# Optimization experiments

Hardware: AMD Instinct MI355X
Metric: run time of the kernel (lower is better)

## Reference

```python
import jax, jax.numpy as jnp
import numpy as np

B, JX, JM, D, H = 8, 2048, 2048, 512, 512
NEG_INF = -1e30


def setup_inputs() -> dict:
    key = jax.random.key(0)
    ks = jax.random.split(key, 6)
    inputs = jax.random.normal(ks[0], (B, JX, D), dtype=jnp.float32)
    memory = jax.random.normal(ks[1], (B, JM, D), dtype=jnp.float32)
    mask = jax.random.randint(ks[2], (B, JM), 0, 2, dtype=jnp.int32)
    # guarantee at least one valid memory slot per row
    mask = mask.at[:, 0].set(1)
    Wq = jax.random.normal(ks[3], (D, H), dtype=jnp.float32) * 0.05
    Wk = jax.random.normal(ks[4], (D, H), dtype=jnp.float32) * 0.05
    Wg = jax.random.normal(ks[5], (2 * D, 2 * D), dtype=jnp.float32) * 0.05
    return {"inputs": inputs, "memory": memory, "mask": mask,
            "Wq": Wq, "Wk": Wk, "Wg": Wg}


def reference(inputs, memory, mask, Wq, Wk, Wg):
    hidden = Wq.shape[-1]
    # two ReLU projections (no bias)
    q = jax.nn.relu(jnp.einsum('bxd,dh->bxh', inputs, Wq))   # [B,JX,H]
    k = jax.nn.relu(jnp.einsum('bmd,dh->bmh', memory, Wk))   # [B,JM,H]
    # scaled dot-product scores
    scores = jnp.einsum('bxh,bmh->bxm', q, k) / (hidden ** 0.5)  # [B,JX,JM]
    # softmax_mask: -inf where mask == 0 (broadcast over JX instead of tile)
    m = mask[:, None, :].astype(scores.dtype)                 # [B,1,JM]
    scores = scores * m + (1.0 - m) * NEG_INF
    logits = jax.nn.softmax(scores, axis=-1)                  # [B,JX,JM]
    # attend over RAW memory (not projected)
    att = jnp.einsum('bxm,bmd->bxd', logits, memory)          # [B,JX,D]
    # gate combiner: concat -> dense(sigmoid, no bias) -> multiply
    res = jnp.concatenate([inputs, att], axis=-1)             # [B,JX,2D]
    g = jax.nn.sigmoid(jnp.einsum('bxe,ef->bxf', res, Wg))
    return res * g
```

## Files before the change

kernel.cpp:

```cpp
#include <hip/hip_runtime.h>

typedef unsigned short u16;
typedef unsigned int   u32;

typedef short s16x8 __attribute__((ext_vector_type(8)));
typedef float f32x4 __attribute__((ext_vector_type(4)));

static __device__ __forceinline__ u16 f2bf(float f) {
  u32 u = __float_as_uint(f);
  u = (u + 0x7fffu + ((u >> 16) & 1u)) >> 16;
  return (u16)u;
}
static __device__ __forceinline__ float bf2f(u16 h) {
  return __uint_as_float(((u32)h) << 16);
}
static __device__ __forceinline__ f32x4 mfma16(s16x8 a, s16x8 b, f32x4 c) {
  return __builtin_amdgcn_mfma_f32_16x16x32_bf16(a, b, c, 0, 0, 0);
}
static __device__ __forceinline__ void gload16(const u16* g, u16* l) {
  __builtin_amdgcn_global_load_lds(
      (const __attribute__((address_space(1))) void*)g,
      (__attribute__((address_space(3))) void*)l, 16, 0, 0);
}

__global__ __launch_bounds__(256) void cvt_k(const float* __restrict__ in,
                                             u16* __restrict__ out, int n8) {
  int i = blockIdx.x * 256 + threadIdx.x;
  if (i >= n8) return;
  const float4* p = reinterpret_cast<const float4*>(in);
  float4 a = p[2 * i], b = p[2 * i + 1];
  union { u16 u[8]; uint4 v; } r;
  r.u[0] = f2bf(a.x); r.u[1] = f2bf(a.y); r.u[2] = f2bf(a.z); r.u[3] = f2bf(a.w);
  r.u[4] = f2bf(b.x); r.u[5] = f2bf(b.y); r.u[6] = f2bf(b.z); r.u[7] = f2bf(b.w);
  reinterpret_cast<uint4*>(out)[i] = r.v;
}

__global__ void tcvt_k(const float* __restrict__ in, u16* __restrict__ out,
                       int R, int C, long long ibs, long long obs) {
  __shared__ float t[32][33];
  const float* ip = in + (size_t)blockIdx.z * ibs;
  u16* op = out + (size_t)blockIdx.z * obs;
  int r0 = blockIdx.y * 32, c0 = blockIdx.x * 32;
  int x = threadIdx.x, y = threadIdx.y;
  for (int i = y; i < 32; i += 8) t[i][x] = ip[(size_t)(r0 + i) * C + c0 + x];
  __syncthreads();
  for (int i = y; i < 32; i += 8) op[(size_t)(c0 + i) * R + r0 + x] = f2bf(t[x][i]);
}

__global__ __launch_bounds__(256) void softmax_k(u16* __restrict__ P,
                                                 const int* __restrict__ mask,
                                                 float scale) {
  __shared__ float redm[4], reds[4];
  const int row = blockIdx.x;
  const int bb = row >> 11;
  const int tid = threadIdx.x;
  u16* p = P + (size_t)row * 2048;
  const int* mk = mask + (size_t)bb * 2048;
  uint4 raw = reinterpret_cast<const uint4*>(p)[tid];
  int4 ma = reinterpret_cast<const int4*>(mk)[2 * tid];
  int4 mc = reinterpret_cast<const int4*>(mk)[2 * tid + 1];
  float v[8];
  v[0] = ma.x ? bf2f((u16)(raw.x & 0xffff)) * scale : -1e30f;
  v[1] = ma.y ? bf2f((u16)(raw.x >> 16))    * scale : -1e30f;
  v[2] = ma.z ? bf2f((u16)(raw.y & 0xffff)) * scale : -1e30f;
  v[3] = ma.w ? bf2f((u16)(raw.y >> 16))    * scale : -1e30f;
  v[4] = mc.x ? bf2f((u16)(raw.z & 0xffff)) * scale : -1e30f;
  v[5] = mc.y ? bf2f((u16)(raw.z >> 16))    * scale : -1e30f;
  v[6] = mc.z ? bf2f((u16)(raw.w & 0xffff)) * scale : -1e30f;
  v[7] = mc.w ? bf2f((u16)(raw.w >> 16))    * scale : -1e30f;
  float mx = v[0];
  #pragma unroll
  for (int i = 1; i < 8; ++i) mx = fmaxf(mx, v[i]);
  for (int off = 32; off; off >>= 1) mx = fmaxf(mx, __shfl_xor(mx, off));
  if ((tid & 63) == 0) redm[tid >> 6] = mx;
  __syncthreads();
  mx = fmaxf(fmaxf(redm[0], redm[1]), fmaxf(redm[2], redm[3]));
  float sum = 0.f;
  #pragma unroll
  for (int i = 0; i < 8; ++i) { v[i] = __expf(v[i] - mx); sum += v[i]; }
  for (int off = 32; off; off >>= 1) sum += __shfl_xor(sum, off);
  if ((tid & 63) == 0) reds[tid >> 6] = sum;
  __syncthreads();
  sum = reds[0] + reds[1] + reds[2] + reds[3];
  float inv = 1.0f / sum;
  union { u16 u[8]; uint4 q; } r;
  #pragma unroll
  for (int i = 0; i < 8; ++i) r.u[i] = f2bf(v[i] * inv);
  reinterpret_cast<uint4*>(p)[tid] = r.q;
}

template <int EPI, int NT, int NX, int NY,
          int LDA, int LDB, int LDC, int KSPLIT, int MSPLIT,
          long long ABS, long long BBS, long long CBS, int NWG>
__global__ __launch_bounds__(256) void g128(
    const u16* __restrict__ A, const u16* __restrict__ A2,
    const u16* __restrict__ Bt, const u16* __restrict__ Bt2,
    float* __restrict__ Cf, u16* __restrict__ Cb,
    const float* __restrict__ R0, const u16* __restrict__ R1) {
  __shared__ u16 As[128 * 64];
  __shared__ u16 Bs[128 * 64];
  const int bid = blockIdx.x;
  const int wgid = (bid & 7) * (NWG / 8) + (bid >> 3);
  const int bx = wgid % NX;
  const int by = (wgid / NX) % NY;
  const int bz = wgid / (NX * NY);
  const int tid = threadIdx.x;
  const int wave = tid >> 6, lane = tid & 63;
  const int m0 = by * 128, n0 = bx * 128;
  const int wr = wave >> 1, wc = wave & 1;
  const int l15 = lane & 15, l4 = lane >> 4;
  const int srow = lane >> 3;
  const int scolsw = (((lane & 7) ^ (lane >> 3)) << 3);
  const int rsw = (l15 & 7) << 3;
  const u16* Bbase = ((m0 < MSPLIT) ? Bt : Bt2) + (size_t)bz * BBS;

  f32x4 acc[4][4];
  #pragma unroll
  for (int i = 0; i < 4; ++i)
    #pragma unroll
    for (int j = 0; j < 4; ++j) acc[i][j] = (f32x4){0.f, 0.f, 0.f, 0.f};

  for (int t = 0; t < NT; ++t) {
    const int k0 = t * 64;
    const u16* Ab;
    int kl;
    if (k0 < KSPLIT) { Ab = A + (size_t)bz * ABS;  kl = k0; }
    else             { Ab = A2 + (size_t)bz * ABS; kl = k0 - KSPLIT; }
    __syncthreads();
    #pragma unroll
    for (int c = 0; c < 4; ++c) {
      int chunk = wave * 4 + c;
      int row = chunk * 8 + srow;
      gload16(Ab + (size_t)(m0 + row) * LDA + kl + scolsw, &As[chunk * 512]);
      gload16(Bbase + (size_t)(n0 + row) * LDB + k0 + scolsw, &Bs[chunk * 512]);
    }
    __syncthreads();
    #pragma unroll
    for (int kk = 0; kk < 64; kk += 32) {
      s16x8 af[4], bfr[4];
      #pragma unroll
      for (int mi = 0; mi < 4; ++mi)
        af[mi] = *reinterpret_cast<const s16x8*>(
            &As[(wr * 64 + mi * 16 + l15) * 64 + ((kk + l4 * 8) ^ rsw)]);
      #pragma unroll
      for (int ni = 0; ni < 4; ++ni)
        bfr[ni] = *reinterpret_cast<const s16x8*>(
            &Bs[(wc * 64 + ni * 16 + l15) * 64 + ((kk + l4 * 8) ^ rsw)]);
      #pragma unroll
      for (int mi = 0; mi < 4; ++mi)
        #pragma unroll
        for (int ni = 0; ni < 4; ++ni)
          acc[mi][ni] = mfma16(af[mi], bfr[ni], acc[mi][ni]);
    }
  }

  #pragma unroll
  for (int mi = 0; mi < 4; ++mi) {
    #pragma unroll
    for (int ni = 0; ni < 4; ++ni) {
      int col = n0 + wc * 64 + ni * 16 + l15;
      #pragma unroll
      for (int j = 0; j < 4; ++j) {
        int row = m0 + wr * 64 + mi * 16 + l4 * 4 + j;
        float v = acc[mi][ni][j];
        size_t cidx = (size_t)bz * CBS + (size_t)row * LDC + col;
        if (EPI == 0) {
          Cb[cidx] = f2bf(fmaxf(v, 0.f));
        } else if (EPI == 1) {
          Cb[cidx] = f2bf(v);
        } else {
          float r = (col < 512) ? R0[(size_t)row * 512 + col]
                                : bf2f(R1[(size_t)row * 512 + (col - 512)]);
          float g = 1.0f / (1.0f + __expf(-v));
          Cf[cidx] = r * g;
        }
      }
    }
  }
}

__global__ __launch_bounds__(256, 2) void gemm_pm_k(const u16* __restrict__ P,
                                                    const u16* __restrict__ MT,
                                                    u16* __restrict__ C) {
  __shared__ u16 As[2][128 * 64];
  __shared__ u16 Bs[2][128 * 64];
  const int l = blockIdx.x;
  const int logical = (l & 7) * 64 + (l >> 3);
  const int n0 = (logical & 3) * 128;
  const int m0 = ((logical >> 2) & 15) * 128;
  const int z = logical >> 6;
  const u16* Ab = P + (size_t)z * 2048 * 2048;
  const u16* Bb = MT + (size_t)z * 512 * 2048;
  u16* Cb = C + (size_t)z * 2048 * 512;
  const int tid = threadIdx.x, wave = tid >> 6, lane = tid & 63;
  const int wr = wave >> 1, wc = wave & 1;
  const int l15 = lane & 15, l4 = lane >> 4;
  const int srow = lane >> 3;
  const int scolsw = (((lane & 7) ^ (lane >> 3)) << 3);
  const int rsw = (l15 & 7) << 3;

  f32x4 acc[4][4];
  #pragma unroll
  for (int i = 0; i < 4; ++i)
    #pragma unroll
    for (int j = 0; j < 4; ++j) acc[i][j] = (f32x4){0.f, 0.f, 0.f, 0.f};

  auto stage = [&](int buf, int k0) {
    #pragma unroll
    for (int c = 0; c < 4; ++c) {
      int chunk = wave * 4 + c;
      int row = chunk * 8 + srow;
      gload16(Ab + (size_t)(m0 + row) * 2048 + k0 + scolsw, &As[buf][chunk * 512]);
      gload16(Bb + (size_t)(n0 + row) * 2048 + k0 + scolsw, &Bs[buf][chunk * 512]);
    }
  };
  auto compute = [&](int cur) {
    __builtin_amdgcn_s_setprio(1);
    #pragma unroll
    for (int kk = 0; kk < 64; kk += 32) {
      s16x8 af[4], bfr[4];
      #pragma unroll
      for (int mi = 0; mi < 4; ++mi)
        af[mi] = *reinterpret_cast<const s16x8*>(
            &As[cur][(wr * 64 + mi * 16 + l15) * 64 + (((kk + l4 * 8) ^ rsw))]);
      #pragma unroll
      for (int ni = 0; ni < 4; ++ni)
        bfr[ni] = *reinterpret_cast<const s16x8*>(
            &Bs[cur][(wc * 64 + ni * 16 + l15) * 64 + (((kk + l4 * 8) ^ rsw))]);
      #pragma unroll
      for (int mi = 0; mi < 4; ++mi)
        #pragma unroll
        for (int ni = 0; ni < 4; ++ni)
          acc[mi][ni] = mfma16(af[mi], bfr[ni], acc[mi][ni]);
    }
    __builtin_amdgcn_s_setprio(0);
  };

  const int nt = 32;
  stage(0, 0);
  stage(1, 64);
  asm volatile("s_waitcnt vmcnt(8)" ::: "memory");
  __builtin_amdgcn_s_barrier();
  for (int t = 0; t < nt; ++t) {
    const int cur = t & 1;
    compute(cur);
    __builtin_amdgcn_s_barrier();
    if (t + 2 < nt) stage(cur, (t + 2) * 64);
    if (t + 1 < nt) {
      if (t + 2 < nt) { asm volatile("s_waitcnt vmcnt(8)" ::: "memory"); }
      else            { asm volatile("s_waitcnt vmcnt(0)" ::: "memory"); }
      __builtin_amdgcn_s_barrier();
    }
  }

  #pragma unroll
  for (int mi = 0; mi < 4; ++mi) {
    #pragma unroll
    for (int ni = 0; ni < 4; ++ni) {
      int col = n0 + wc * 64 + ni * 16 + l15;
      #pragma unroll
      for (int j = 0; j < 4; ++j) {
        int row = m0 + wr * 64 + mi * 16 + l4 * 4 + j;
        Cb[(size_t)row * 512 + col] = f2bf(acc[mi][ni][j]);
      }
    }
  }
}

extern "C" void kernel_launch(void* const* d_in, const int* in_sizes, int n_in,
                              void* d_out, int out_size, void* d_ws, size_t ws_size,
                              hipStream_t stream) {
  const float* inputs = (const float*)d_in[0];
  const float* memory = (const float*)d_in[1];
  const int*   mask   = (const int*)d_in[2];
  const float* Wq     = (const float*)d_in[3];
  const float* Wk     = (const float*)d_in[4];
  const float* Wg     = (const float*)d_in[5];
  float* out = (float*)d_out;

  char* ws = (char*)d_ws;
  size_t off = 0;
  auto alloc = [&](size_t bytes) {
    void* p = ws + off;
    off += (bytes + 255) & ~(size_t)255;
    return p;
  };
  u16* in_b  = (u16*)alloc(16384ULL * 512 * 2);
  u16* mem_b = (u16*)alloc(16384ULL * 512 * 2);
  u16* memT  = (u16*)alloc(16384ULL * 512 * 2);
  u16* WqT   = (u16*)alloc(512ULL * 512 * 2);
  u16* WkT   = (u16*)alloc(512ULL * 512 * 2);
  u16* WgT   = (u16*)alloc(1024ULL * 1024 * 2);
  u16* q_b   = (u16*)alloc(16384ULL * 512 * 2);
  u16* k_b   = (u16*)alloc(16384ULL * 512 * 2);
  u16* sc    = (u16*)alloc(8ULL * 2048 * 2048 * 2);
  u16* att_b = (u16*)alloc(16384ULL * 512 * 2);
  (void)ws_size; (void)in_sizes; (void)n_in; (void)out_size; (void)mem_b;

  const int n8 = (16384 * 512) / 8;
  cvt_k<<<(n8 + 255) / 256, 256, 0, stream>>>(inputs, in_b, n8);
  cvt_k<<<(n8 + 255) / 256, 256, 0, stream>>>(memory, in_b + 16384ULL * 512, n8);
  dim3 tb(32, 8);
  tcvt_k<<<dim3(16, 16, 1), tb, 0, stream>>>(Wq, WqT, 512, 512, 0, 0);
  tcvt_k<<<dim3(16, 16, 1), tb, 0, stream>>>(Wk, WkT, 512, 512, 0, 0);
  tcvt_k<<<dim3(32, 32, 1), tb, 0, stream>>>(Wg, WgT, 1024, 1024, 0, 0);
  tcvt_k<<<dim3(16, 64, 8), tb, 0, stream>>>(memory, memT, 2048, 512,
                                             2048LL * 512, 2048LL * 512);

  g128<0, 8, 4, 256, 512, 512, 512, (1 << 30), 16384, 0, 0, 0, 1024>
      <<<1024, 256, 0, stream>>>(in_b, nullptr, WqT, WkT,
                                 nullptr, q_b, nullptr, nullptr);

  g128<1, 8, 16, 16, 512, 512, 2048, (1 << 30), (1 << 30),
       2048LL * 512, 2048LL * 512, 2048LL * 2048, 2048>
      <<<2048, 256, 0, stream>>>(q_b, nullptr, k_b, k_b,
                                 nullptr, sc, nullptr, nullptr);

  softmax_k<<<16384, 256, 0, stream>>>(sc, mask, 0.044194173824159216f);

  gemm_pm_k<<<512, 256, 0, stream>>>(sc, memT, att_b);

  g128<3, 16, 8, 128, 512, 1024, 1024, 512, (1 << 30), 0, 0, 0, 1024>
      <<<1024, 256, 0, stream>>>(in_b, att_b, WgT, WgT,
                                 out, nullptr, inputs, att_b);
}
```

Before: 268.4 us.

## Unify GEMMs into double-buffered kernel with LDS-staged vectorized epilogue

Replaces the single-buffered g128 GEMM with a double-buffered variant (the same prefetch/vmcnt scheme previously used only in gemm_pm_k) and routes all four GEMMs, including the P·M product, through it. Global loads for tile t+2 now overlap with MFMA work on tile t. The epilogue goes through LDS so each thread writes 16 contiguous outputs with vector stores, replacing the scattered scalar stores. The LDS staging adds extra barriers in the epilogue, and the doubled shared-memory footprint may limit occupancy.

```diff
diff --git a/kernel.cpp b/kernel.cpp
--- a/kernel.cpp
+++ b/kernel.cpp
@@ -22,6 +22,15 @@
       (const __attribute__((address_space(1))) void*)g,
       (__attribute__((address_space(3))) void*)l, 16, 0, 0);
 }
+
+#define WAITVM8() asm volatile("s_waitcnt vmcnt(8)" ::: "memory")
+#define WAITVM0() asm volatile("s_waitcnt vmcnt(0)" ::: "memory")
+#define BAR()                                  \
+  do {                                         \
+    asm volatile("" ::: "memory");             \
+    __builtin_amdgcn_s_barrier();              \
+    asm volatile("" ::: "memory");             \
+  } while (0)
 
 __global__ __launch_bounds__(256) void cvt_k(const float* __restrict__ in,
                                              u16* __restrict__ out, int n8) {
@@ -92,13 +101,13 @@
 template <int EPI, int NT, int NX, int NY,
           int LDA, int LDB, int LDC, int KSPLIT, int MSPLIT,
           long long ABS, long long BBS, long long CBS, int NWG>
-__global__ __launch_bounds__(256) void g128(
+__global__ __launch_bounds__(256, 2) void gdb(
     const u16* __restrict__ A, const u16* __restrict__ A2,
     const u16* __restrict__ Bt, const u16* __restrict__ Bt2,
     float* __restrict__ Cf, u16* __restrict__ Cb,
     const float* __restrict__ R0, const u16* __restrict__ R1) {
-  __shared__ u16 As[128 * 64];
-  __shared__ u16 Bs[128 * 64];
+  __shared__ u16 As[2][128 * 64];
+  __shared__ u16 Bs[2][128 * 64];
   const int bid = blockIdx.x;
   const int wgid = (bid & 7) * (NWG / 8) + (bid >> 3);
   const int bx = wgid % NX;
@@ -113,6 +122,8 @@
   const int scolsw = (((lane & 7) ^ (lane >> 3)) << 3);
   const int rsw = (l15 & 7) << 3;
   const u16* Bbase = ((m0 < MSPLIT) ? Bt : Bt2) + (size_t)bz * BBS;
+  const u16* Abase0 = A + (size_t)bz * ABS;
+  const u16* Abase1 = A2 + (size_t)bz * ABS;
 
   f32x4 acc[4][4];
   #pragma unroll
@@ -120,149 +131,105 @@
     #pragma unroll
     for (int j = 0; j < 4; ++j) acc[i][j] = (f32x4){0.f, 0.f, 0.f, 0.f};
 
-  for (int t = 0; t < NT; ++t) {
-    const int k0 = t * 64;
+  auto stage = [&](int buf, int k0) {
     const u16* Ab;
     int kl;
-    if (k0 < KSPLIT) { Ab = A + (size_t)bz * ABS;  kl = k0; }
-    else             { Ab = A2 + (size_t)bz * ABS; kl = k0 - KSPLIT; }
-    __syncthreads();
+    if (k0 < KSPLIT) { Ab = Abase0; kl = k0; }
+    else             { Ab = Abase1; kl = k0 - KSPLIT; }
     #pragma unroll
     for (int c = 0; c < 4; ++c) {
       int chunk = wave * 4 + c;
       int row = chunk * 8 + srow;
-      gload16(Ab + (size_t)(m0 + row) * LDA + kl + scolsw, &As[chunk * 512]);
-      gload16(Bbase + (size_t)(n0 + row) * LDB + k0 + scolsw, &Bs[chunk * 512]);
-    }
-    __syncthreads();
+      gload16(Ab + (size_t)(m0 + row) * LDA + kl + scolsw, &As[buf][chunk * 512]);
+      gload16(Bbase + (size_t)(n0 + row) * LDB + k0 + scolsw, &Bs[buf][chunk * 512]);
+    }
+  };
+  auto compute = [&](int cur) {
+    __builtin_amdgcn_s_setprio(1);
     #pragma unroll
     for (int kk = 0; kk < 64; kk += 32) {
       s16x8 af[4], bfr[4];
       #pragma unroll
       for (int mi = 0; mi < 4; ++mi)
         af[mi] = *reinterpret_cast<const s16x8*>(
-            &As[(wr * 64 + mi * 16 + l15) * 64 + ((kk + l4 * 8) ^ rsw)]);
+            &As[cur][(wr * 64 + mi * 16 + l15) * 64 + ((kk + l4 * 8) ^ rsw)]);
       #pragma unroll
       for (int ni = 0; ni < 4; ++ni)
         bfr[ni] = *reinterpret_cast<const s16x8*>(
-            &Bs[(wc * 64 + ni * 16 + l15) * 64 + ((kk + l4 * 8) ^ rsw)]);
+            &Bs[cur][(wc * 64 + ni * 16 + l15) * 64 + ((kk + l4 * 8) ^ rsw)]);
       #pragma unroll
       for (int mi = 0; mi < 4; ++mi)
         #pragma unroll
         for (int ni = 0; ni < 4; ++ni)
           acc[mi][ni] = mfma16(af[mi], bfr[ni], acc[mi][ni]);
     }
+    __builtin_amdgcn_s_setprio(0);
+  };
+
+  stage(0, 0);
+  stage(1, 64);
+  WAITVM8();
+  BAR();
+  for (int t = 0; t < NT; ++t) {
+    const int cur = t & 1;
+    compute(cur);
+    BAR();
+    if (t + 2 < NT) stage(cur, (t + 2) * 64);
+    if (t + 1 < NT) {
+      if (t + 2 < NT) { WAITVM8(); } else { WAITVM0(); }
+      BAR();
+    }
   }
 
+  float* LF = (float*)(&As[0][0]);
+  const int er = tid >> 3;
+  const int ec = (tid & 7) * 16;
   #pragma unroll
   for (int mi = 0; mi < 4; ++mi) {
+    __syncthreads();
     #pragma unroll
     for (int ni = 0; ni < 4; ++ni) {
-      int col = n0 + wc * 64 + ni * 16 + l15;
-      #pragma unroll
-      for (int j = 0; j < 4; ++j) {
-        int row = m0 + wr * 64 + mi * 16 + l4 * 4 + j;
-        float v = acc[mi][ni][j];
-        size_t cidx = (size_t)bz * CBS + (size_t)row * LDC + col;
-        if (EPI == 0) {
-          Cb[cidx] = f2bf(fmaxf(v, 0.f));
-        } else if (EPI == 1) {
-          Cb[cidx] = f2bf(v);
-        } else {
-          float r = (col < 512) ? R0[(size_t)row * 512 + col]
-                                : bf2f(R1[(size_t)row * 512 + (col - 512)]);
-          float g = 1.0f / (1.0f + __expf(-v));
-          Cf[cidx] = r * g;
+      int lcol = wc * 64 + ni * 16 + l15;
+      #pragma unroll
+      for (int j = 0; j < 4; ++j)
+        LF[(wr * 16 + l4 * 4 + j) * 132 + lcol] = acc[mi][ni][j];
+    }
+    __syncthreads();
+    int grow = m0 + mi * 16 + (er & 15) + (er >> 4) * 64;
+    int gcol = n0 + ec;
+    float v[16];
+    #pragma unroll
+    for (int i = 0; i < 4; ++i)
+      *reinterpret_cast<f32x4*>(&v[4 * i]) =
+          *reinterpret_cast<const f32x4*>(&LF[er * 132 + ec + 4 * i]);
+    if (EPI == 3) {
+      float* o = Cf + (size_t)bz * CBS + (size_t)grow * LDC + gcol;
+      if (n0 < 512) {
+        const float* r0 = R0 + (size_t)grow * 512 + gcol;
+        #pragma unroll
+        for (int i = 0; i < 16; ++i) {
+          float g = 1.0f / (1.0f + __expf(-v[i]));
+          v[i] = r0[i] * g;
+        }
+      } else {
+        const u16* r1 = R1 + (size_t)grow * 512 + (gcol - 512);
+        #pragma unroll
+        for (int i = 0; i < 16; ++i) {
+          float g = 1.0f / (1.0f + __expf(-v[i]));
+          v[i] = bf2f(r1[i]) * g;
         }
       }
-    }
-  }
-}
-
-__global__ __launch_bounds__(256, 2) void gemm_pm_k(const u16* __restrict__ P,
-                                                    const u16* __restrict__ MT,
-                                                    u16* __restrict__ C) {
-  __shared__ u16 As[2][128 * 64];
-  __shared__ u16 Bs[2][128 * 64];
-  const int l = blockIdx.x;
-  const int logical = (l & 7) * 64 + (l >> 3);
-  const int n0 = (logical & 3) * 128;
-  const int m0 = ((logical >> 2) & 15) * 128;
-  const int z = logical >> 6;
-  const u16* Ab = P + (size_t)z * 2048 * 2048;
-  const u16* Bb = MT + (size_t)z * 512 * 2048;
-  u16* Cb = C + (size_t)z * 2048 * 512;
-  const int tid = threadIdx.x, wave = tid >> 6, lane = tid & 63;
-  const int wr = wave >> 1, wc = wave & 1;
-  const int l15 = lane & 15, l4 = lane >> 4;
-  const int srow = lane >> 3;
-  const int scolsw = (((lane & 7) ^ (lane >> 3)) << 3);
-  const int rsw = (l15 & 7) << 3;
-
-  f32x4 acc[4][4];
-  #pragma unroll
-  for (int i = 0; i < 4; ++i)
-    #pragma unroll
-    for (int j = 0; j < 4; ++j) acc[i][j] = (f32x4){0.f, 0.f, 0.f, 0.f};
-
-  auto stage = [&](int buf, int k0) {
-    #pragma unroll
-    for (int c = 0; c < 4; ++c) {
-      int chunk = wave * 4 + c;
-      int row = chunk * 8 + srow;
-      gload16(Ab + (size_t)(m0 + row) * 2048 + k0 + scolsw, &As[buf][chunk * 512]);
-      gload16(Bb + (size_t)(n0 + row) * 2048 + k0 + scolsw, &Bs[buf][chunk * 512]);
-    }
-  };
-  auto compute = [&](int cur) {
-    __builtin_amdgcn_s_setprio(1);
-    #pragma unroll
-    for (int kk = 0; kk < 64; kk += 32) {
-      s16x8 af[4], bfr[4];
-      #pragma unroll
-      for (int mi = 0; mi < 4; ++mi)
-        af[mi] = *reinterpret_cast<const s16x8*>(
-            &As[cur][(wr * 64 + mi * 16 + l15) * 64 + (((kk + l4 * 8) ^ rsw))]);
-      #pragma unroll
-      for (int ni = 0; ni < 4; ++ni)
-        bfr[ni] = *reinterpret_cast<const s16x8*>(
-            &Bs[cur][(wc * 64 + ni * 16 + l15) * 64 + (((kk + l4 * 8) ^ rsw))]);
-      #pragma unroll
-      for (int mi = 0; mi < 4; ++mi)
-        #pragma unroll
-        for (int ni = 0; ni < 4; ++ni)
-          acc[mi][ni] = mfma16(af[mi], bfr[ni], acc[mi][ni]);
-    }
-    __builtin_amdgcn_s_setprio(0);
-  };
-
-  const int nt = 32;
-  stage(0, 0);
-  stage(1, 64);
-  asm volatile("s_waitcnt vmcnt(8)" ::: "memory");
-  __builtin_amdgcn_s_barrier();
-  for (int t = 0; t < nt; ++t) {
-    const int cur = t & 1;
-    compute(cur);
-    __builtin_amdgcn_s_barrier();
-    if (t + 2 < nt) stage(cur, (t + 2) * 64);
-    if (t + 1 < nt) {
-      if (t + 2 < nt) { asm volatile("s_waitcnt vmcnt(8)" ::: "memory"); }
-      else            { asm volatile("s_waitcnt vmcnt(0)" ::: "memory"); }
-      __builtin_amdgcn_s_barrier();
-    }
-  }
-
-  #pragma unroll
-  for (int mi = 0; mi < 4; ++mi) {
-    #pragma unroll
-    for (int ni = 0; ni < 4; ++ni) {
-      int col = n0 + wc * 64 + ni * 16 + l15;
-      #pragma unroll
-      for (int j = 0; j < 4; ++j) {
-        int row = m0 + wr * 64 + mi * 16 + l4 * 4 + j;
-        Cb[(size_t)row * 512 + col] = f2bf(acc[mi][ni][j]);
-      }
+      #pragma unroll
+      for (int i = 0; i < 4; ++i)
+        *reinterpret_cast<float4*>(&o[4 * i]) = *reinterpret_cast<float4*>(&v[4 * i]);
+    } else {
+      union { u16 u[16]; uint4 q[2]; } pk;
+      #pragma unroll
+      for (int i = 0; i < 16; ++i)
+        pk.u[i] = f2bf(EPI == 0 ? fmaxf(v[i], 0.f) : v[i]);
+      u16* o = Cb + (size_t)bz * CBS + (size_t)grow * LDC + gcol;
+      reinterpret_cast<uint4*>(o)[0] = pk.q[0];
+      reinterpret_cast<uint4*>(o)[1] = pk.q[1];
     }
   }
 }
@@ -307,20 +274,26 @@
   tcvt_k<<<dim3(16, 64, 8), tb, 0, stream>>>(memory, memT, 2048, 512,
                                              2048LL * 512, 2048LL * 512);
 
-  g128<0, 8, 4, 256, 512, 512, 512, (1 << 30), 16384, 0, 0, 0, 1024>
-      <<<1024, 256, 0, stream>>>(in_b, nullptr, WqT, WkT,
-                                 nullptr, q_b, nullptr, nullptr);
-
-  g128<1, 8, 16, 16, 512, 512, 2048, (1 << 30), (1 << 30),
-       2048LL * 512, 2048LL * 512, 2048LL * 2048, 2048>
-      <<<2048, 256, 0, stream>>>(q_b, nullptr, k_b, k_b,
-                                 nullptr, sc, nullptr, nullptr);
+  const int BIG = 1 << 30;
+
+  gdb<0, 8, 4, 256, 512, 512, 512, (1 << 30), 16384, 0, 0, 0, 1024>
+      <<<1024, 256, 0, stream>>>(in_b, in_b, WqT, WkT, nullptr, q_b,
+                                 nullptr, nullptr);
+
+  gdb<1, 8, 16, 16, 512, 512, 2048, (1 << 30), (1 << 30),
+      2048LL * 512, 2048LL * 512, 2048LL * 2048, 2048>
+      <<<2048, 256, 0, stream>>>(q_b, q_b, k_b, k_b, nullptr, sc,
+                                 nullptr, nullptr);
 
   softmax_k<<<16384, 256, 0, stream>>>(sc, mask, 0.044194173824159216f);
 
-  gemm_pm_k<<<512, 256, 0, stream>>>(sc, memT, att_b);
-
-  g128<3, 16, 8, 128, 512, 1024, 1024, 512, (1 << 30), 0, 0, 0, 1024>
-      <<<1024, 256, 0, stream>>>(in_b, att_b, WgT, WgT,
-                                 out, nullptr, inputs, att_b);
-}
+  gdb<1, 32, 4, 16, 2048, 2048, 512, (1 << 30), (1 << 30),
+      2048LL * 2048, 512LL * 2048, 2048LL * 512, 512>
+      <<<512, 256, 0, stream>>>(sc, sc, memT, memT, nullptr, att_b,
+                                nullptr, nullptr);
+
+  gdb<3, 16, 8, 128, 512, 1024, 1024, 512, (1 << 30), 0, 0, 0, 1024>
+      <<<1024, 256, 0, stream>>>(in_b, att_b, WgT, WgT, out, nullptr,
+                                 inputs, att_b);
+  (void)BIG;
+}
```

Result: faster. 235.5 us (-12.2%).
